# Kernel optimization log

Measured on AMD Instinct MI355X. Metric: run time of the kernel, lower is better.

The kernel has to match this reference:

```python
import jax, jax.numpy as jnp
import numpy as np

# static config matching init_kwargs
IN_SIZE = 128
OUT_SIZE = 128
KSIZE = 3
POS = 10
DIL = 1
B = 8
L = 8192


def setup_inputs() -> dict:
    key = jax.random.key(0)
    k1, k2, k3, k4, k5 = jax.random.split(key, 5)
    inputs = jax.random.normal(k1, (B, IN_SIZE, L), dtype=jnp.float32)
    connections = jax.random.randint(k2, (B, L), 0, L)  # indices into length axis
    mask = jax.random.randint(k3, (B, L), 0, 2).astype(bool)
    ch_in = (2 * IN_SIZE + POS) * KSIZE  # 798
    W = jax.random.normal(k4, (OUT_SIZE, ch_in), dtype=jnp.float32) / np.float32(np.sqrt(ch_in))
    b = jax.random.normal(k5, (OUT_SIZE,), dtype=jnp.float32) * 0.01
    return {"inputs": inputs, "connections": connections, "mask": mask, "W": W, "b": b}


def reference(inputs, connections, mask, W, b):
    Bn, C, Ln = inputs.shape
    # gather neighbor features: out[b,c,l] = inputs[b,c,connections[b,l]]  -> [B,C,L]
    conn_vals = jnp.take_along_axis(inputs, connections[:, None, :], axis=2)
    # trig positional encoding of relative offsets  -> [B,POS,L]
    pos = jnp.arange(Ln, dtype=jnp.float32)[None]              # [1,L]
    delta = (pos - connections.astype(jnp.float32))[:, None, :]  # [B,1,L]
    scales = (2.0 ** jnp.arange(POS, dtype=jnp.float32))[None, :, None]
    penc = jnp.sin(scales * delta / 1000.0)
    out = jnp.concatenate([inputs, conn_vals, penc], axis=1)   # [B, 2C+POS, L]
    # non-causal pad + unfold (window KSIZE, step 1); num windows == L
    pad = KSIZE * DIL // 2
    out = jnp.pad(out, ((0, 0), (0, 0), (pad, pad)))
    # build [B, Ch, KSIZE, L]: window k is out_padded[..., k : k+L]
    out = jnp.stack([out[..., k:k + Ln] for k in range(KSIZE)], axis=2)
    out = out.reshape(Bn, -1, Ln)                               # [B, Ch*KSIZE, L]
    # 1x1 conv == per-position GEMM
    y = jnp.einsum('oc,bcl->bol', W, out) + b[None, :, None]    # [B, OUT, L]
    return y * mask[:, None, :].astype(y.dtype)
```

## Files before the change

kernel.cpp:

```cpp
#include <hip/hip_runtime.h>
#include <math.h>

#define B_    8
#define C_    128
#define L_    8192
#define O_    128
#define POS_  10
#define CHIN  798
#define CH_   266
#define GSTR  128
#define NCH   9
#define TL2   128
#define G_ELEMS  ((size_t)B_ * L_ * GSTR)
#define WT_ELEMS ((size_t)3 * NCH * O_ * 32)

typedef _Float16 half8 __attribute__((ext_vector_type(8)));
typedef short short8 __attribute__((ext_vector_type(8)));
typedef float f32x4  __attribute__((ext_vector_type(4)));

__device__ __forceinline__ void detect_core(const uint4* __restrict__ m,
                                            int* __restrict__ mflag, int tid) {
    __shared__ int s[2];
    if (tid < 2) s[tid] = 0;
    __syncthreads();
    unsigned sub = 0, mid = 0;
    #pragma unroll
    for (int k = 0; k < 16; ++k) {
        uint4 w = m[tid + k * 256];
        sub |= (w.x | w.y | w.z | w.w) & 0xFFFFFF00u;
        mid |= (w.y | w.w) & 0x000000FFu;
    }
    unsigned long long bs = __ballot(sub != 0);
    unsigned long long bm = __ballot(mid != 0);
    if ((tid & 63) == 0) {
        if (bs) atomicOr(&s[0], 1);
        if (bm) atomicOr(&s[1], 1);
    }
    __syncthreads();
    if (tid == 0) mflag[0] = s[0] ? 1 : (s[1] ? 0 : 2);
}

__global__ void detect_kernel(const uint4* __restrict__ m, int* __restrict__ mflag) {
    detect_core(m, mflag, threadIdx.x);
}

__global__ __launch_bounds__(256, 4)
void prep_kernel(const float* __restrict__ inputs, const float* __restrict__ W,
                 const uint4* __restrict__ maskv,
                 _Float16* __restrict__ G, _Float16* __restrict__ Wt2,
                 int* __restrict__ mflag) {
    __shared__ float tile[64][65];
    const int bid = blockIdx.x;
    const int tid = threadIdx.x;

    if (bid == 2480) { detect_core(maskv, mflag, tid); return; }

    if (bid >= 2048) {
        int idx = (bid - 2048) * 256 + tid;
        int cc  = idx & 31;
        int o   = (idx >> 5) & 127;
        int tch = idx >> 12;
        int ch  = tch % 9;
        int t   = tch / 9;
        int cg  = ch * 32 + cc;
        Wt2[idx] = (cg < CH_) ? (_Float16)W[o * CHIN + 3 * cg + t] : (_Float16)0.f;
        return;
    }

    const int b  = bid & 7;
    const int r  = bid >> 3;
    const int c0 = (r & 1) * 64;
    const int l0 = (r >> 1) * 64;
    const int ty = tid >> 6, tx = tid & 63;

    #pragma unroll
    for (int it = 0; it < 16; ++it) {
        int cl = it * 4 + ty;
        tile[cl][tx] = inputs[((size_t)(b * C_ + c0 + cl)) * L_ + l0 + tx];
    }
    __syncthreads();
    const int cp = (tid & 31) * 2;
    const int lr = tid >> 5;
    #pragma unroll
    for (int it = 0; it < 8; ++it) {
        int ll = it * 8 + lr;
        _Float16 pair[2] = {(_Float16)tile[cp][ll], (_Float16)tile[cp + 1][ll]};
        *(unsigned*)&G[((size_t)(b * L_ + l0 + ll)) * GSTR + c0 + cp] = *(unsigned*)pair;
    }
}

__global__ __launch_bounds__(256)
void k2_gemm(const _Float16* __restrict__ G, const _Float16* __restrict__ Wt2,
             const int* __restrict__ conn,
             const unsigned char* __restrict__ mask,
             const float* __restrict__ bias,
             float* __restrict__ out,
             const int* __restrict__ mflag_p) {
    __shared__ _Float16 As[2][128][104];
    __shared__ _Float16 Bs[2][130][40];
    __shared__ int conn_s[130];

    const int bid = blockIdx.x;
    const int b   = bid & 7;
    const int l0  = (bid >> 3) * TL2;
    const int tid  = threadIdx.x;
    const int wave = tid >> 6;
    const int lane = tid & 63;
    const int wo = wave & 1;
    const int wl = wave >> 1;
    const int g  = lane >> 4;
    const int ln = lane & 15;

    const _Float16* gb = G + (size_t)b * L_ * GSTR;

    for (int j = tid; j < TL2 + 2; j += 256) {
        int l_ = l0 - 1 + j;
        conn_s[j] = ((unsigned)l_ < (unsigned)L_) ? conn[b * L_ + l_] : 0;
    }

    auto aloadg = [&](int ch, int q) -> short8 {
        int cb = q & 3, o = (q >> 2) & 127, tp = q >> 9;
        return *(const short8*)&Wt2[((size_t)((tp * NCH + ch) * O_ + o)) * 32 + cb * 8];
    };
    auto bloadg = [&](int ch, int q) -> short8 {
        int cb = q & 3, j = q >> 2;
        int l_ = l0 - 1 + j;
        short8 v = (short8)0;
        if ((unsigned)l_ < (unsigned)L_) {
            if (ch < 4) {
                v = *(const short8*)&gb[(size_t)l_ * GSTR + ch * 32 + cb * 8];
            } else if (ch < 8) {
                int cj = conn_s[j];
                v = *(const short8*)&gb[(size_t)cj * GSTR + (ch - 4) * 32 + cb * 8];
            } else if (cb < 2) {
                float d = (float)(l_ - conn_s[j]);
                _Float16 h[8];
                #pragma unroll
                for (int e = 0; e < 8; ++e) {
                    int p = cb * 8 + e;
                    h[e] = (p < POS_) ? (_Float16)sinf(((float)(1 << p)) * d / 1000.0f)
                                      : (_Float16)0.f;
                }
                v = *(short8*)h;
            }
        }
        return v;
    };

#define ALOADG(CH) { a0 = aloadg((CH), tid);        a1 = aloadg((CH), tid + 256); \
                     a2 = aloadg((CH), tid + 512);  a3 = aloadg((CH), tid + 768); \
                     a4 = aloadg((CH), tid + 1024); a5 = aloadg((CH), tid + 1280); }

#define AWR1(V, Q, BUF) { int cb_ = (Q) & 3, o_ = ((Q) >> 2) & 127, tp_ = (Q) >> 9; \
        *(short8*)&As[BUF][o_][tp_ * 32 + cb_ * 8] = V; }

#define AWR(BUF) { AWR1(a0, tid, BUF) AWR1(a1, tid + 256, BUF) \
                   AWR1(a2, tid + 512, BUF) AWR1(a3, tid + 768, BUF) \
                   AWR1(a4, tid + 1024, BUF) AWR1(a5, tid + 1280, BUF) }

#define BLOADG(CH) { s0 = bloadg((CH), tid); s1 = bloadg((CH), tid + 256); \
        if (tid < 8) s2 = bloadg((CH), 512 + tid); }

#define BWR1(V, Q, BUF) { int cb_ = (Q) & 3, j_ = (Q) >> 2; \
        *(short8*)&Bs[BUF][j_][cb_ * 8] = V; }

#define BWR(BUF) { BWR1(s0, tid, BUF) BWR1(s1, tid + 256, BUF) \
        if (tid < 8) { BWR1(s2, 512 + tid, BUF) } }

#define COMPUTE(BUF) { _Pragma("unroll") for (int t_ = 0; t_ < 3; ++t_) { \
        half8 bf_[4]; \
        _Pragma("unroll") for (int n_ = 0; n_ < 4; ++n_) \
            bf_[n_] = *(const half8*)&Bs[BUF][wl * 64 + n_ * 16 + ln + t_][8 * g]; \
        _Pragma("unroll") for (int m_ = 0; m_ < 4; ++m_) { \
            half8 af_ = *(const half8*)&As[BUF][wo * 64 + m_ * 16 + ln][t_ * 32 + 8 * g]; \
            _Pragma("unroll") for (int n_ = 0; n_ < 4; ++n_) \
                acc[m_][n_] = __builtin_amdgcn_mfma_f32_16x16x32_f16(af_, bf_[n_], acc[m_][n_], 0, 0, 0); } } }

    f32x4 acc[4][4];
    #pragma unroll
    for (int m = 0; m < 4; ++m)
        #pragma unroll
        for (int n = 0; n < 4; ++n) acc[m][n] = (f32x4)0.f;

    short8 a0, a1, a2, a3, a4, a5, s0, s1, s2;

    ALOADG(0); BLOADG(0);
    AWR(0); BWR(0);
    __syncthreads();

    for (int ch = 0; ch < 8; ch += 2) {
        ALOADG(ch + 1); BLOADG(ch + 1);
        COMPUTE(0);
        AWR(1); BWR(1);
        __syncthreads();

        ALOADG(ch + 2); BLOADG(ch + 2);
        COMPUTE(1);
        AWR(0); BWR(0);
        __syncthreads();
    }
    COMPUTE(0);

    const int mflag = mflag_p[0];
    float mv[4];
    #pragma unroll
    for (int n = 0; n < 4; ++n) {
        int l = l0 + wl * 64 + n * 16 + ln;
        int idx = b * L_ + l;
        if (mflag == 1)      mv[n] = mask[idx] ? 1.f : 0.f;
        else if (mflag == 0) mv[n] = ((const int*)mask)[idx] ? 1.f : 0.f;
        else                 mv[n] = ((const int*)mask)[2 * idx] ? 1.f : 0.f;
    }
    #pragma unroll
    for (int m = 0; m < 4; ++m) {
        #pragma unroll
        for (int r = 0; r < 4; ++r) {
            int o = wo * 64 + m * 16 + g * 4 + r;
            float bo = bias[o];
            #pragma unroll
            for (int n = 0; n < 4; ++n) {
                int l = l0 + wl * 64 + n * 16 + ln;
                out[((size_t)(b * O_ + o)) * L_ + l] = (acc[m][n][r] + bo) * mv[n];
            }
        }
    }
#undef ALOADG
#undef AWR1
#undef AWR
#undef BLOADG
#undef BWR1
#undef BWR
#undef COMPUTE
}

__global__ __launch_bounds__(256, 2)
void cc_fallback_kernel(const float* __restrict__ inputs,
                        const int* __restrict__ conn,
                        const unsigned char* __restrict__ mask,
                        const float* __restrict__ W,
                        const float* __restrict__ bias,
                        float* __restrict__ out,
                        const int* __restrict__ mflag_p) {
    __shared__ int   conn_s[130];
    __shared__ float feat_s[16][132];
    __shared__ float Ws[48][136];

    const int b   = blockIdx.y;
    const int l0  = blockIdx.x * 128;
    const int tid = threadIdx.x;
    const int ot  = tid >> 4;
    const int lt  = tid & 15;
    const int o0  = ot * 8;
    const int ll  = lt * 8;

    for (int j = tid; j < 130; j += 256) {
        int lg = l0 - 1 + j;
        conn_s[j] = ((unsigned)lg < (unsigned)L_) ? conn[b * L_ + lg] : -1;
    }
    float acc[8][8];
    #pragma unroll
    for (int i = 0; i < 8; ++i)
        #pragma unroll
        for (int j = 0; j < 8; ++j) acc[i][j] = 0.f;

    const int tc = ot, tj = lt;
    for (int chunk = 0; chunk < 17; ++chunk) {
        const int CN  = (chunk < 16) ? 16 : POS_;
        const int cg0 = chunk * 16;
        const int col0 = 3 * cg0;
        __syncthreads();
        {
            const int nw = O_ * CN * 3;
            for (int idx = tid; idx < nw; idx += 256) {
                int o = idx & 127, kk = idx >> 7;
                Ws[kk][o] = W[o * CHIN + col0 + kk];
            }
        }
        if (chunk < 8) {
            const float* src = inputs + ((size_t)b * C_ + (cg0 + tc)) * L_;
            for (int j = tj; j < 130; j += 16) {
                int lg = l0 - 1 + j;
                feat_s[tc][j] = ((unsigned)lg < (unsigned)L_) ? src[lg] : 0.f;
            }
        } else if (chunk < 16) {
            const float* src = inputs + ((size_t)b * C_ + (cg0 - 128 + tc)) * L_;
            for (int j = tj; j < 130; j += 16) {
                int cj = conn_s[j];
                feat_s[tc][j] = (cj >= 0) ? src[cj] : 0.f;
            }
        } else if (tc < POS_) {
            const float sc = (float)(1 << tc);
            for (int j = tj; j < 130; j += 16) {
                int cj = conn_s[j];
                int lg = l0 - 1 + j;
                float v = 0.f;
                if (cj >= 0) v = sinf((sc * (float)(lg - cj)) / 1000.0f);
                feat_s[tc][j] = v;
            }
        }
        __syncthreads();
        for (int c = 0; c < CN; ++c) {
            float f[10];
            float4 fa = *(const float4*)&feat_s[c][ll];
            float4 fb = *(const float4*)&feat_s[c][ll + 4];
            float2 fc2 = *(const float2*)&feat_s[c][ll + 8];
            f[0]=fa.x; f[1]=fa.y; f[2]=fa.z; f[3]=fa.w;
            f[4]=fb.x; f[5]=fb.y; f[6]=fb.z; f[7]=fb.w;
            f[8]=fc2.x; f[9]=fc2.y;
            #pragma unroll
            for (int k = 0; k < 3; ++k) {
                const float* wrow = &Ws[c * 3 + k][o0];
                float4 wa = *(const float4*)&wrow[0];
                float4 wb = *(const float4*)&wrow[4];
                float w[8] = {wa.x, wa.y, wa.z, wa.w, wb.x, wb.y, wb.z, wb.w};
                #pragma unroll
                for (int oi = 0; oi < 8; ++oi)
                    #pragma unroll
                    for (int li = 0; li < 8; ++li)
                        acc[oi][li] = fmaf(w[oi], f[li + k], acc[oi][li]);
            }
        }
    }
    const int mflag = mflag_p[0];
    const int lbase = l0 + ll;
    float mv[8];
    #pragma unroll
    for (int li = 0; li < 8; ++li) {
        int idx = b * L_ + lbase + li;
        if (mflag == 1)      mv[li] = mask[idx] ? 1.f : 0.f;
        else if (mflag == 0) mv[li] = ((const int*)mask)[idx] ? 1.f : 0.f;
        else                 mv[li] = ((const int*)mask)[2 * idx] ? 1.f : 0.f;
    }
    #pragma unroll
    for (int oi = 0; oi < 8; ++oi) {
        float bo = bias[o0 + oi];
        float* dst = out + ((size_t)b * O_ + o0 + oi) * L_ + lbase;
        #pragma unroll
        for (int li = 0; li < 8; ++li) dst[li] = (acc[oi][li] + bo) * mv[li];
    }
}

extern "C" void kernel_launch(void* const* d_in, const int* in_sizes, int n_in,
                              void* d_out, int out_size, void* d_ws, size_t ws_size,
                              hipStream_t stream) {
    const float*         inputs = (const float*)d_in[0];
    const int*           conn   = (const int*)d_in[1];
    const unsigned char* mask   = (const unsigned char*)d_in[2];
    const float*         W      = (const float*)d_in[3];
    const float*         bias   = (const float*)d_in[4];
    float*               out    = (float*)d_out;

    const size_t g_bytes  = G_ELEMS * sizeof(_Float16);
    const size_t wt_bytes = WT_ELEMS * sizeof(_Float16);
    const size_t need     = g_bytes + wt_bytes + 64;

    if (ws_size < need) {
        int* mflag = (int*)d_ws;
        detect_kernel<<<1, 256, 0, stream>>>((const uint4*)mask, mflag);
        dim3 grid(L_ / 128, B_);
        cc_fallback_kernel<<<grid, 256, 0, stream>>>(inputs, conn, mask, W, bias, out, mflag);
        return;
    }

    _Float16* G     = (_Float16*)d_ws;
    _Float16* Wt2   = (_Float16*)((char*)d_ws + g_bytes);
    int*      mflag = (int*)((char*)d_ws + g_bytes + wt_bytes);

    prep_kernel<<<2481, 256, 0, stream>>>(inputs, W, (const uint4*)mask, G, Wt2, mflag);
    k2_gemm<<<512, 256, 0, stream>>>(G, Wt2, conn, mask, bias, out, mflag);
}
```

Measured before the change: 45.24 us.

## Stage GEMM A and B tiles with direct global-to-LDS DMA loads

Replaces the register-staged global loads and LDS stores for the weight (A) and input/gathered (B) tiles with `global_load_lds` 16-byte direct transfers. The LDS layout is reorganised into unpadded 32-wide rows so each wave's 64 lanes fill 16 contiguous rows. Only the halo rows and the positional-encoding chunk still go through registers. This is meant to cut VGPR pressure and LDS write instructions, but the removed padding may add LDS bank conflicts on the MFMA fragment reads. It also relies on the barrier correctly waiting for the asynchronous LDS writes to finish.

Measured after the change: 51.43 us. 13.7% more time.

```diff
diff --git a/kernel.cpp b/kernel.cpp
--- a/kernel.cpp
+++ b/kernel.cpp
@@ -18,6 +18,13 @@
 typedef short short8 __attribute__((ext_vector_type(8)));
 typedef float f32x4  __attribute__((ext_vector_type(4)));
 
+typedef __attribute__((address_space(3))) unsigned       lds_uint;
+typedef __attribute__((address_space(1))) const unsigned gl_uint;
+
+__device__ __forceinline__ void dma16(const _Float16* g, _Float16* l) {
+    __builtin_amdgcn_global_load_lds((gl_uint*)g, (lds_uint*)l, 16, 0, 0);
+}
+
 __device__ __forceinline__ void detect_core(const uint4* __restrict__ m,
                                             int* __restrict__ mflag, int tid) {
     __shared__ int s[2];
@@ -96,8 +103,8 @@
              const float* __restrict__ bias,
              float* __restrict__ out,
              const int* __restrict__ mflag_p) {
-    __shared__ _Float16 As[2][128][104];
-    __shared__ _Float16 Bs[2][130][40];
+    __shared__ _Float16 As[2][3][128][32];
+    __shared__ _Float16 Bs[2][130][32];
     __shared__ int conn_s[130];
 
     const int bid = blockIdx.x;
@@ -118,61 +125,97 @@
         conn_s[j] = ((unsigned)l_ < (unsigned)L_) ? conn[b * L_ + l_] : 0;
     }
 
-    auto aloadg = [&](int ch, int q) -> short8 {
-        int cb = q & 3, o = (q >> 2) & 127, tp = q >> 9;
-        return *(const short8*)&Wt2[((size_t)((tp * NCH + ch) * O_ + o)) * 32 + cb * 8];
+    const int ra  = 1 + 32 * wave + (lane >> 2);
+    const int cja = conn[b * L_ + l0 - 1 + ra];
+    const int cjb = conn[b * L_ + l0 - 1 + ra + 16];
+    const int cbl = lane & 3;
+
+    auto stage_dma = [&](int ch, int buf) {
+        #pragma unroll
+        for (int i = 0; i < 6; ++i) {
+            int ap = 6 * wave + i;
+            int tp = ap >> 3;
+            int og = ap & 7;
+            int o  = og * 16 + (lane >> 2);
+            const _Float16* src = &Wt2[((size_t)((tp * NCH + ch) * O_ + o)) * 32 + cbl * 8];
+            dma16(src, &As[buf][tp][og * 16][0]);
+        }
+        #pragma unroll
+        for (int i = 0; i < 2; ++i) {
+            int r0 = 1 + 32 * wave + 16 * i;
+            const _Float16* src;
+            if (ch < 4) {
+                int r = r0 + (lane >> 2);
+                src = &gb[(size_t)(l0 - 1 + r) * GSTR + ch * 32 + cbl * 8];
+            } else {
+                int cj = i ? cjb : cja;
+                src = &gb[(size_t)cj * GSTR + (ch - 4) * 32 + cbl * 8];
+            }
+            dma16(src, &Bs[buf][r0][0]);
+        }
     };
-    auto bloadg = [&](int ch, int q) -> short8 {
+    auto stage_dma_a_only = [&](int ch, int buf) {
+        #pragma unroll
+        for (int i = 0; i < 6; ++i) {
+            int ap = 6 * wave + i;
+            int tp = ap >> 3;
+            int og = ap & 7;
+            int o  = og * 16 + (lane >> 2);
+            const _Float16* src = &Wt2[((size_t)((tp * NCH + ch) * O_ + o)) * 32 + cbl * 8];
+            dma16(src, &As[buf][tp][og * 16][0]);
+        }
+    };
+
+    auto halo_load = [&](int ch) -> short8 {
+        int row = (tid >> 2) ? 129 : 0;
+        int l_  = l0 - 1 + row;
+        short8 v = (short8)0;
+        if ((unsigned)l_ < (unsigned)L_) {
+            if (ch < 4) {
+                v = *(const short8*)&gb[(size_t)l_ * GSTR + ch * 32 + (tid & 3) * 8];
+            } else {
+                int cj = conn_s[row];
+                v = *(const short8*)&gb[(size_t)cj * GSTR + (ch - 4) * 32 + (tid & 3) * 8];
+            }
+        }
+        return v;
+    };
+    auto halo_write = [&](short8 v, int buf) {
+        int row = (tid >> 2) ? 129 : 0;
+        *(short8*)&Bs[buf][row][(tid & 3) * 8] = v;
+    };
+
+    auto penc_val = [&](int q) -> short8 {
         int cb = q & 3, j = q >> 2;
         int l_ = l0 - 1 + j;
         short8 v = (short8)0;
-        if ((unsigned)l_ < (unsigned)L_) {
-            if (ch < 4) {
-                v = *(const short8*)&gb[(size_t)l_ * GSTR + ch * 32 + cb * 8];
-            } else if (ch < 8) {
-                int cj = conn_s[j];
-                v = *(const short8*)&gb[(size_t)cj * GSTR + (ch - 4) * 32 + cb * 8];
-            } else if (cb < 2) {
-                float d = (float)(l_ - conn_s[j]);
-                _Float16 h[8];
-                #pragma unroll
-                for (int e = 0; e < 8; ++e) {
-                    int p = cb * 8 + e;
-                    h[e] = (p < POS_) ? (_Float16)sinf(((float)(1 << p)) * d / 1000.0f)
-                                      : (_Float16)0.f;
-                }
-                v = *(short8*)h;
-            }
+        if ((unsigned)l_ < (unsigned)L_ && cb < 2) {
+            float d = (float)(l_ - conn_s[j]);
+            _Float16 h[8];
+            #pragma unroll
+            for (int e = 0; e < 8; ++e) {
+                int p = cb * 8 + e;
+                h[e] = (p < POS_) ? (_Float16)sinf(((float)(1 << p)) * d / 1000.0f)
+                                  : (_Float16)0.f;
+            }
+            v = *(short8*)h;
         }
         return v;
     };
 
-#define ALOADG(CH) { a0 = aloadg((CH), tid);        a1 = aloadg((CH), tid + 256); \
-                     a2 = aloadg((CH), tid + 512);  a3 = aloadg((CH), tid + 768); \
-                     a4 = aloadg((CH), tid + 1024); a5 = aloadg((CH), tid + 1280); }
-
-#define AWR1(V, Q, BUF) { int cb_ = (Q) & 3, o_ = ((Q) >> 2) & 127, tp_ = (Q) >> 9; \
-        *(short8*)&As[BUF][o_][tp_ * 32 + cb_ * 8] = V; }
-
-#define AWR(BUF) { AWR1(a0, tid, BUF) AWR1(a1, tid + 256, BUF) \
-                   AWR1(a2, tid + 512, BUF) AWR1(a3, tid + 768, BUF) \
-                   AWR1(a4, tid + 1024, BUF) AWR1(a5, tid + 1280, BUF) }
-
-#define BLOADG(CH) { s0 = bloadg((CH), tid); s1 = bloadg((CH), tid + 256); \
-        if (tid < 8) s2 = bloadg((CH), 512 + tid); }
-
-#define BWR1(V, Q, BUF) { int cb_ = (Q) & 3, j_ = (Q) >> 2; \
-        *(short8*)&Bs[BUF][j_][cb_ * 8] = V; }
-
-#define BWR(BUF) { BWR1(s0, tid, BUF) BWR1(s1, tid + 256, BUF) \
-        if (tid < 8) { BWR1(s2, 512 + tid, BUF) } }
+#define PENC_WR(BUF) { { int cb_ = tid & 3, j_ = tid >> 2; \
+            *(short8*)&Bs[BUF][j_][cb_ * 8] = s0; } \
+        { int q_ = tid + 256; int cb_ = q_ & 3, j_ = q_ >> 2; \
+            *(short8*)&Bs[BUF][j_][cb_ * 8] = s1; } \
+        if (tid < 8) { int q_ = 512 + tid; int cb_ = q_ & 3, j_ = q_ >> 2; \
+            *(short8*)&Bs[BUF][j_][cb_ * 8] = s2; } }
 
 #define COMPUTE(BUF) { _Pragma("unroll") for (int t_ = 0; t_ < 3; ++t_) { \
         half8 bf_[4]; \
         _Pragma("unroll") for (int n_ = 0; n_ < 4; ++n_) \
             bf_[n_] = *(const half8*)&Bs[BUF][wl * 64 + n_ * 16 + ln + t_][8 * g]; \
         _Pragma("unroll") for (int m_ = 0; m_ < 4; ++m_) { \
-            half8 af_ = *(const half8*)&As[BUF][wo * 64 + m_ * 16 + ln][t_ * 32 + 8 * g]; \
+            half8 af_ = *(const half8*)&As[BUF][t_][wo * 64 + m_ * 16 + ln][8 * g]; \
             _Pragma("unroll") for (int n_ = 0; n_ < 4; ++n_) \
                 acc[m_][n_] = __builtin_amdgcn_mfma_f32_16x16x32_f16(af_, bf_[n_], acc[m_][n_], 0, 0, 0); } } }
 
@@ -182,21 +225,31 @@
         #pragma unroll
         for (int n = 0; n < 4; ++n) acc[m][n] = (f32x4)0.f;
 
-    short8 a0, a1, a2, a3, a4, a5, s0, s1, s2;
-
-    ALOADG(0); BLOADG(0);
-    AWR(0); BWR(0);
+    short8 s0, s1, s2, hv;
+
+    stage_dma(0, 0);
+    if (tid < 8) { hv = halo_load(0); halo_write(hv, 0); }
     __syncthreads();
 
     for (int ch = 0; ch < 8; ch += 2) {
-        ALOADG(ch + 1); BLOADG(ch + 1);
+        stage_dma(ch + 1, 1);
+        if (tid < 8) hv = halo_load(ch + 1);
         COMPUTE(0);
-        AWR(1); BWR(1);
+        if (tid < 8) halo_write(hv, 1);
         __syncthreads();
 
-        ALOADG(ch + 2); BLOADG(ch + 2);
-        COMPUTE(1);
-        AWR(0); BWR(0);
+        if (ch + 2 == 8) {
+            stage_dma_a_only(8, 0);
+            s0 = penc_val(tid); s1 = penc_val(tid + 256);
+            if (tid < 8) s2 = penc_val(512 + tid);
+            COMPUTE(1);
+            PENC_WR(0);
+        } else {
+            stage_dma(ch + 2, 0);
+            if (tid < 8) hv = halo_load(ch + 2);
+            COMPUTE(1);
+            if (tid < 8) halo_write(hv, 0);
+        }
         __syncthreads();
     }
     COMPUTE(0);
@@ -224,12 +277,7 @@
             }
         }
     }
-#undef ALOADG
-#undef AWR1
-#undef AWR
-#undef BLOADG
-#undef BWR1
-#undef BWR
+#undef PENC_WR
 #undef COMPUTE
 }
 
```
